# Performance work log

Measured on AMD Instinct MI355X. Metric: run time of the kernel, lower is better.

## Reference

```python
import jax, jax.numpy as jnp
import numpy as np

NUM_HEADS = 12
LN_EPS = 1e-5


def setup_inputs() -> dict:
    key = jax.random.key(0)
    k1, k2, k3 = jax.random.split(key, 3)
    B, S, E = 8, 1024, 768
    x = jax.random.normal(k1, (B, S, E), dtype=jnp.float32)
    # torch nn.Linear(E, 3E): y = x @ W.T + b. We store the transposed weight [E, 3E].
    w_qkv = jax.random.normal(k2, (E, 3 * E), dtype=jnp.float32) * (1.0 / np.sqrt(E))
    b_qkv = jax.random.normal(k3, (3 * E,), dtype=jnp.float32) * 0.02
    ln_gamma = jnp.ones((E,), dtype=jnp.float32)
    ln_beta = jnp.zeros((E,), dtype=jnp.float32)
    return {"x": x, "w_qkv": w_qkv, "b_qkv": b_qkv, "ln_gamma": ln_gamma, "ln_beta": ln_beta}


def reference(x, w_qkv, b_qkv, ln_gamma, ln_beta):
    B, S, E = x.shape
    H = NUM_HEADS
    D = E // H
    qkv = x @ w_qkv + b_qkv                       # [B, S, 3E]
    qkv = qkv.reshape(B, S, 3, H, D)
    q, k, v = qkv[:, :, 0], qkv[:, :, 1], qkv[:, :, 2]   # each [B, S, H, D]
    scores = jnp.einsum("bshd,bthd->bhst", q, k) / jnp.sqrt(jnp.float32(D))
    attn = jax.nn.softmax(scores, axis=-1)        # [B, H, S, S]
    out = jnp.einsum("bhst,bthd->bshd", attn, v)  # [B, S, H, D]
    # per-head concat in head order == reshape to [B, S, E]
    out = out.reshape(B, S, E)
    y = x + out
    mean = jnp.mean(y, axis=-1, keepdims=True)
    var = jnp.var(y, axis=-1, keepdims=True)
    y = (y - mean) * jax.lax.rsqrt(var + LN_EPS)
    return y * ln_gamma + ln_beta
```

## Files before the change

kernel.cpp:

```cpp
#include <hip/hip_runtime.h>

typedef __attribute__((ext_vector_type(8))) short short8;
typedef __attribute__((ext_vector_type(4))) float f32x4;

#define DEVI __device__ __forceinline__

DEVI unsigned fbits(float f) { return __builtin_bit_cast(unsigned, f); }
DEVI unsigned short f2bf(float f) {
    unsigned u = __builtin_bit_cast(unsigned, f);
    u += 0x7fffu + ((u >> 16) & 1u);
    return (unsigned short)(u >> 16);
}
DEVI unsigned pktrunc(float a, float b) {
    return __builtin_amdgcn_perm(fbits(b), fbits(a), 0x07060302u);
}
DEVI void async16(const unsigned short* g, unsigned short* l) {
    __builtin_amdgcn_global_load_lds(
        (const __attribute__((address_space(1))) void*)g,
        (__attribute__((address_space(3))) void*)l,
        16, 0, 0);
}
#define BAR()    asm volatile("s_barrier" ::: "memory")
#define WAITV4() asm volatile("s_waitcnt vmcnt(4)" ::: "memory")
#define WAITV0() asm volatile("s_waitcnt vmcnt(0)" ::: "memory")

__global__ __launch_bounds__(256) void kcvt(const float* __restrict__ x,
                                            unsigned short* __restrict__ xb) {
    const int i = (blockIdx.x * 256 + threadIdx.x) * 4;
    const float4 v = *(const float4*)&x[i];
    uint2 pk;
    pk.x = (unsigned)f2bf(v.x) | ((unsigned)f2bf(v.y) << 16);
    pk.y = (unsigned)f2bf(v.z) | ((unsigned)f2bf(v.w) << 16);
    *(uint2*)&xb[i] = pk;
}

__global__ void ktrans(const float* __restrict__ w,
                       unsigned short* __restrict__ wt) {
    __shared__ float t[32][33];
    const int tx = threadIdx.x, ty = threadIdx.y;
    const int n0 = blockIdx.x * 32, k0 = blockIdx.y * 32;
#pragma unroll
    for (int i = 0; i < 4; i++)
        t[ty + i * 8][tx] = w[(k0 + ty + i * 8) * 2304 + n0 + tx];
    __syncthreads();
#pragma unroll
    for (int i = 0; i < 4; i++)
        wt[(n0 + ty + i * 8) * 768 + k0 + tx] = f2bf(t[tx][ty + i * 8]);
}

__global__ __launch_bounds__(256) void kgemm(
        const unsigned short* __restrict__ xb,
        const unsigned short* __restrict__ wt,
        const float* __restrict__ bias,
        unsigned short* __restrict__ q,
        unsigned short* __restrict__ k_,
        unsigned short* __restrict__ vt) {
    __shared__ __align__(16) unsigned short As[3][8 * 512];
    __shared__ __align__(16) unsigned short Bs[3][8 * 512];
    const int tid = threadIdx.x;
    const int w = tid >> 6, lane = tid & 63;
    const int wm = w >> 1, wn = w & 1;
    const int m0 = blockIdx.y * 128, n0 = blockIdx.x * 128;
    const int gr = lane & 15, gc = (lane >> 4) * 8;

    f32x4 acc[4][4] = {};

    auto issue = [&](int kk, int b) {
#pragma unroll
        for (int j = 0; j < 2; j++) {
            const int t = w + j * 4;
            async16(&xb[(m0 + t * 16 + gr) * 768 + kk + gc], &As[b][t * 512]);
            async16(&wt[(n0 + t * 16 + gr) * 768 + kk + gc], &Bs[b][t * 512]);
        }
    };

    issue(0, 0);
    issue(32, 1);

    for (int it = 0; it < 24; it++) {
        const int cur = it % 3;
        if (it < 23) { WAITV4(); } else { WAITV0(); }
        BAR();
        if (it + 2 < 24) issue((it + 2) * 32, (it + 2) % 3);

        short8 af[4], bf[4];
#pragma unroll
        for (int mi = 0; mi < 4; mi++)
            af[mi] = *(const short8*)&As[cur][(wm * 4 + mi) * 512 + lane * 8];
#pragma unroll
        for (int ni = 0; ni < 4; ni++)
            bf[ni] = *(const short8*)&Bs[cur][(wn * 4 + ni) * 512 + lane * 8];
#pragma unroll
        for (int mi = 0; mi < 4; mi++)
#pragma unroll
            for (int ni = 0; ni < 4; ni++)
                acc[mi][ni] = __builtin_amdgcn_mfma_f32_16x16x32_bf16(
                    af[mi], bf[ni], acc[mi][ni], 0, 0, 0);
    }

    const int col0 = n0 + wn * 64;
    const int row0 = m0 + wm * 64;
#pragma unroll
    for (int mi = 0; mi < 4; mi++) {
#pragma unroll
        for (int ni = 0; ni < 4; ni++) {
            const int n_ = col0 + ni * 16 + (lane & 15);
            const float bv = bias[n_];
            const int which = n_ / 768;
            const int r7 = n_ % 768;
            const int h = r7 >> 6, d = r7 & 63;
#pragma unroll
            for (int r = 0; r < 4; r++) {
                const int m_ = row0 + mi * 16 + (lane >> 4) * 4 + r;
                const int bb = m_ >> 10, s = m_ & 1023;
                const int bh = bb * 12 + h;
                const unsigned short o = f2bf(acc[mi][ni][r] + bv);
                if (which == 0)      q[(bh * 1024 + s) * 64 + d] = o;
                else if (which == 1) k_[(bh * 1024 + s) * 64 + d] = o;
                else                 vt[(bh * 64 + d) * 1024 + s] = o;
            }
        }
    }
}

#define SCL 0.18033688011112042f

__global__ __launch_bounds__(256) void kattn(
        const unsigned short* __restrict__ q,
        const unsigned short* __restrict__ k_,
        const unsigned short* __restrict__ vt,
        float* __restrict__ out) {
    __shared__ __align__(16) unsigned short Ks[2][8 * 512];
    __shared__ __align__(16) unsigned short Vs[2][8 * 512];
    __shared__ __align__(16) unsigned short Ps[4][4 * 512];
    const int tid = threadIdx.x;
    const int w = tid >> 6, lane = tid & 63;
    const int bh = blockIdx.x;
    const int qt = blockIdx.y;
    const int bb = bh / 12, h = bh % 12;
    const unsigned short* qb = q + bh * 1024 * 64;
    const unsigned short* kb = k_ + bh * 1024 * 64;
    const unsigned short* vb = vt + bh * 64 * 1024;

    const int frow = lane & 15;
    const int grp = lane >> 4;
    const int m0 = qt * 128 + w * 32;

    auto issue = [&](int t0, int b) {
#pragma unroll
        for (int j = 0; j < 2; j++) {
            const int t = w * 2 + j, ti = t >> 1, ks = t & 1;
            async16(&kb[(t0 + ti * 16 + frow) * 64 + ks * 32 + grp * 8], &Ks[b][t * 512]);
            async16(&vb[(ti * 16 + frow) * 1024 + t0 + ks * 32 + grp * 8], &Vs[b][t * 512]);
        }
    };

    short8 qf[2][2];
#pragma unroll
    for (int mi = 0; mi < 2; mi++)
#pragma unroll
        for (int ks = 0; ks < 2; ks++)
            qf[mi][ks] = *(const short8*)&qb[(m0 + mi * 16 + frow) * 64 + ks * 32 + grp * 8];

    issue(0, 0);

    f32x4 oacc[2][4] = {};
    float rmax[2] = {-INFINITY, -INFINITY}, rsum[2] = {0.f, 0.f};

    for (int tt = 0; tt < 16; tt++) {
        const int cur = tt & 1;
        WAITV0();
        BAR();
        if (tt + 1 < 16) issue((tt + 1) * 64, cur ^ 1);

        f32x4 sacc[4][2] = {};
#pragma unroll
        for (int ks = 0; ks < 2; ks++) {
            short8 kf[4];
#pragma unroll
            for (int ni = 0; ni < 4; ni++)
                kf[ni] = *(const short8*)&Ks[cur][(ni * 2 + ks) * 512 + lane * 8];
#pragma unroll
            for (int ni = 0; ni < 4; ni++)
#pragma unroll
                for (int mi = 0; mi < 2; mi++)
                    sacc[ni][mi] = __builtin_amdgcn_mfma_f32_16x16x32_bf16(
                        kf[ni], qf[mi][ks], sacc[ni][mi], 0, 0, 0);
        }

#pragma unroll
        for (int mi = 0; mi < 2; mi++) {
            float mt = -INFINITY;
#pragma unroll
            for (int ni = 0; ni < 4; ni++)
#pragma unroll
                for (int r = 0; r < 4; r++) mt = fmaxf(mt, sacc[ni][mi][r]);
            mt = fmaxf(mt, __shfl_xor(mt, 16, 64));
            mt = fmaxf(mt, __shfl_xor(mt, 32, 64));
            const float mnew = fmaxf(rmax[mi], mt);
            const float alpha = exp2f((rmax[mi] - mnew) * SCL);
            rmax[mi] = mnew;
            const float mb = mnew * SCL;
            float ps = 0.f;
#pragma unroll
            for (int ni = 0; ni < 4; ni++)
#pragma unroll
                for (int r = 0; r < 4; r++) {
                    const float p = exp2f(sacc[ni][mi][r] * SCL - mb);
                    sacc[ni][mi][r] = p;
                    ps += p;
                }
            ps += __shfl_xor(ps, 16, 64);
            ps += __shfl_xor(ps, 32, 64);
            rsum[mi] = rsum[mi] * alpha + ps;
#pragma unroll
            for (int di = 0; di < 4; di++) oacc[mi][di] *= alpha;
#pragma unroll
            for (int ni = 0; ni < 4; ni++) {
                uint2 pk;
                pk.x = pktrunc(sacc[ni][mi][0], sacc[ni][mi][1]);
                pk.y = pktrunc(sacc[ni][mi][2], sacc[ni][mi][3]);
                const int dlane = frow + (((ni << 1) + (grp >> 1)) & 3) * 16;
                *(uint2*)&Ps[w][(mi * 2 + (ni >> 1)) * 512 + dlane * 8 + (grp & 1) * 4] = pk;
            }
        }

#pragma unroll
        for (int ks = 0; ks < 2; ks++) {
            short8 vf[4], pf[2];
#pragma unroll
            for (int di = 0; di < 4; di++)
                vf[di] = *(const short8*)&Vs[cur][(di * 2 + ks) * 512 + lane * 8];
#pragma unroll
            for (int mi = 0; mi < 2; mi++)
                pf[mi] = *(const short8*)&Ps[w][(mi * 2 + ks) * 512 + lane * 8];
#pragma unroll
            for (int mi = 0; mi < 2; mi++)
#pragma unroll
                for (int di = 0; di < 4; di++)
                    oacc[mi][di] = __builtin_amdgcn_mfma_f32_16x16x32_bf16(
                        vf[di], pf[mi], oacc[mi][di], 0, 0, 0);
        }
    }

#pragma unroll
    for (int mi = 0; mi < 2; mi++) {
        const float inv = 1.0f / rsum[mi];
        const int s = m0 + mi * 16 + frow;
#pragma unroll
        for (int di = 0; di < 4; di++) {
            f32x4 o = oacc[mi][di] * inv;
            const int d0 = di * 16 + grp * 4;
            *(f32x4*)&out[(bb * 1024 + s) * 768 + h * 64 + d0] = o;
        }
    }
}

__global__ __launch_bounds__(256) void kln(
        const float* __restrict__ x,
        const float* __restrict__ gamma,
        const float* __restrict__ beta,
        float* __restrict__ out) {
    __shared__ float red[8];
    const int row = blockIdx.x;
    const int tid = threadIdx.x;
    const float* xr = x + row * 768;
    float* orow = out + row * 768;
    float y[3], sum = 0.f, sumsq = 0.f;
#pragma unroll
    for (int i = 0; i < 3; i++) {
        const int e = tid + i * 256;
        const float v = xr[e] + orow[e];
        y[i] = v; sum += v; sumsq += v * v;
    }
#pragma unroll
    for (int o = 1; o < 64; o <<= 1) {
        sum += __shfl_xor(sum, o, 64);
        sumsq += __shfl_xor(sumsq, o, 64);
    }
    const int w = tid >> 6, lane = tid & 63;
    if (lane == 0) { red[w] = sum; red[4 + w] = sumsq; }
    __syncthreads();
    sum = red[0] + red[1] + red[2] + red[3];
    sumsq = red[4] + red[5] + red[6] + red[7];
    const float mean = sum * (1.0f / 768.0f);
    const float var = sumsq * (1.0f / 768.0f) - mean * mean;
    const float rs = rsqrtf(var + 1e-5f);
#pragma unroll
    for (int i = 0; i < 3; i++) {
        const int e = tid + i * 256;
        orow[e] = (y[i] - mean) * rs * gamma[e] + beta[e];
    }
}

extern "C" void kernel_launch(void* const* d_in, const int* in_sizes, int n_in,
                              void* d_out, int out_size, void* d_ws, size_t ws_size,
                              hipStream_t stream) {
    (void)in_sizes; (void)n_in; (void)out_size; (void)ws_size;
    const float* x     = (const float*)d_in[0];
    const float* wqkv  = (const float*)d_in[1];
    const float* bqkv  = (const float*)d_in[2];
    const float* gamma = (const float*)d_in[3];
    const float* beta  = (const float*)d_in[4];
    float* out = (float*)d_out;
    unsigned short* ws = (unsigned short*)d_ws;

    unsigned short* wt = ws;
    unsigned short* xb = wt + 2304 * 768;
    unsigned short* q  = xb + 8192 * 768;
    unsigned short* k  = q + 96 * 1024 * 64;
    unsigned short* vt = k + 96 * 1024 * 64;

    kcvt<<<6144, 256, 0, stream>>>(x, xb);
    ktrans<<<dim3(72, 24), dim3(32, 8), 0, stream>>>(wqkv, wt);
    kgemm<<<dim3(18, 64), 256, 0, stream>>>(xb, wt, bqkv, q, k, vt);
    kattn<<<dim3(96, 8), 256, 0, stream>>>(q, k, vt, out);
    kln<<<8192, 256, 0, stream>>>(x, gamma, beta, out);
}
```

Measured before the change: 248.9 us.

## Fuse fp32-to-bf16 conversion of x into GEMM and stage V-transpose through LDS

Removes the separate kcvt kernel. The GEMM now loads fp32 x directly into registers, truncates it to bf16 and writes it into LDS, so the x round trip through a bf16 workspace goes away. The pipeline shrinks from triple-buffered async loads to double buffering with register prefetch of A. The V output tile is transposed through LDS so stores to vt are coalesced 16-byte writes instead of scattered 2-byte stores. Conversion switches from round-to-nearest to truncation, which slightly changes numerics, and the shallower pipeline may expose more memory latency.

Result: no change. 253.5 us (+1.8%).

```diff
diff --git a/kernel.cpp b/kernel.cpp
--- a/kernel.cpp
+++ b/kernel.cpp
@@ -21,18 +21,8 @@
         16, 0, 0);
 }
 #define BAR()    asm volatile("s_barrier" ::: "memory")
-#define WAITV4() asm volatile("s_waitcnt vmcnt(4)" ::: "memory")
+#define BARF()   asm volatile("s_waitcnt lgkmcnt(0)\ns_barrier" ::: "memory")
 #define WAITV0() asm volatile("s_waitcnt vmcnt(0)" ::: "memory")
-
-__global__ __launch_bounds__(256) void kcvt(const float* __restrict__ x,
-                                            unsigned short* __restrict__ xb) {
-    const int i = (blockIdx.x * 256 + threadIdx.x) * 4;
-    const float4 v = *(const float4*)&x[i];
-    uint2 pk;
-    pk.x = (unsigned)f2bf(v.x) | ((unsigned)f2bf(v.y) << 16);
-    pk.y = (unsigned)f2bf(v.z) | ((unsigned)f2bf(v.w) << 16);
-    *(uint2*)&xb[i] = pk;
-}
 
 __global__ void ktrans(const float* __restrict__ w,
                        unsigned short* __restrict__ wt) {
@@ -49,14 +39,13 @@
 }
 
 __global__ __launch_bounds__(256) void kgemm(
-        const unsigned short* __restrict__ xb,
+        const float* __restrict__ A,
         const unsigned short* __restrict__ wt,
         const float* __restrict__ bias,
         unsigned short* __restrict__ q,
         unsigned short* __restrict__ k_,
         unsigned short* __restrict__ vt) {
-    __shared__ __align__(16) unsigned short As[3][8 * 512];
-    __shared__ __align__(16) unsigned short Bs[3][8 * 512];
+    __shared__ __align__(16) unsigned short pool[17408];
     const int tid = threadIdx.x;
     const int w = tid >> 6, lane = tid & 63;
     const int wm = w >> 1, wn = w & 1;
@@ -64,60 +53,109 @@
     const int gr = lane & 15, gc = (lane >> 4) * 8;
 
     f32x4 acc[4][4] = {};
-
-    auto issue = [&](int kk, int b) {
+    float4 a0[2], a1[2];
+
+    auto issueB = [&](int kk, int b) {
 #pragma unroll
         for (int j = 0; j < 2; j++) {
             const int t = w + j * 4;
-            async16(&xb[(m0 + t * 16 + gr) * 768 + kk + gc], &As[b][t * 512]);
-            async16(&wt[(n0 + t * 16 + gr) * 768 + kk + gc], &Bs[b][t * 512]);
+            async16(&wt[(n0 + t * 16 + gr) * 768 + kk + gc],
+                    &pool[8192 + b * 4096 + t * 512 + lane * 8]);
         }
     };
-
-    issue(0, 0);
-    issue(32, 1);
+    auto loadA = [&](int kk) {
+#pragma unroll
+        for (int j = 0; j < 2; j++) {
+            const int t = w + j * 4;
+            const float* p = &A[(m0 + t * 16 + gr) * 768 + kk + gc];
+            a0[j] = *(const float4*)p;
+            a1[j] = *(const float4*)(p + 4);
+        }
+    };
+    auto packA = [&](int b) {
+#pragma unroll
+        for (int j = 0; j < 2; j++) {
+            const int t = w + j * 4;
+            uint4 pk;
+            pk.x = pktrunc(a0[j].x, a0[j].y);
+            pk.y = pktrunc(a0[j].z, a0[j].w);
+            pk.z = pktrunc(a1[j].x, a1[j].y);
+            pk.w = pktrunc(a1[j].z, a1[j].w);
+            *(uint4*)&pool[b * 4096 + t * 512 + lane * 8] = pk;
+        }
+    };
+
+    loadA(0); packA(0); issueB(0, 0);
 
     for (int it = 0; it < 24; it++) {
-        const int cur = it % 3;
-        if (it < 23) { WAITV4(); } else { WAITV0(); }
-        BAR();
-        if (it + 2 < 24) issue((it + 2) * 32, (it + 2) % 3);
+        const int cur = it & 1;
+        WAITV0();
+        BARF();
+        if (it < 23) { issueB((it + 1) * 32, cur ^ 1); loadA((it + 1) * 32); }
 
         short8 af[4], bf[4];
 #pragma unroll
         for (int mi = 0; mi < 4; mi++)
-            af[mi] = *(const short8*)&As[cur][(wm * 4 + mi) * 512 + lane * 8];
+            af[mi] = *(const short8*)&pool[cur * 4096 + (wm * 4 + mi) * 512 + lane * 8];
 #pragma unroll
         for (int ni = 0; ni < 4; ni++)
-            bf[ni] = *(const short8*)&Bs[cur][(wn * 4 + ni) * 512 + lane * 8];
+            bf[ni] = *(const short8*)&pool[8192 + cur * 4096 + (wn * 4 + ni) * 512 + lane * 8];
 #pragma unroll
         for (int mi = 0; mi < 4; mi++)
 #pragma unroll
             for (int ni = 0; ni < 4; ni++)
                 acc[mi][ni] = __builtin_amdgcn_mfma_f32_16x16x32_bf16(
                     af[mi], bf[ni], acc[mi][ni], 0, 0, 0);
-    }
-
-    const int col0 = n0 + wn * 64;
-    const int row0 = m0 + wm * 64;
-#pragma unroll
-    for (int mi = 0; mi < 4; mi++) {
-#pragma unroll
-        for (int ni = 0; ni < 4; ni++) {
-            const int n_ = col0 + ni * 16 + (lane & 15);
-            const float bv = bias[n_];
-            const int which = n_ / 768;
-            const int r7 = n_ % 768;
-            const int h = r7 >> 6, d = r7 & 63;
-#pragma unroll
-            for (int r = 0; r < 4; r++) {
-                const int m_ = row0 + mi * 16 + (lane >> 4) * 4 + r;
-                const int bb = m_ >> 10, s = m_ & 1023;
+
+        if (it < 23) packA(cur ^ 1);
+    }
+
+    const int which = n0 / 768;
+    const int bb = m0 >> 10, sbase = m0 & 1023;
+
+    if (which == 2) {
+        BARF();
+#pragma unroll
+        for (int mi = 0; mi < 4; mi++) {
+            const int mloc = wm * 64 + mi * 16 + (lane >> 4) * 4;
+#pragma unroll
+            for (int ni = 0; ni < 4; ni++) {
+                const int nl = wn * 64 + ni * 16 + gr;
+                const float bv = bias[n0 + nl];
+                uint2 pk;
+                pk.x = pktrunc(acc[mi][ni][0] + bv, acc[mi][ni][1] + bv);
+                pk.y = pktrunc(acc[mi][ni][2] + bv, acc[mi][ni][3] + bv);
+                *(uint2*)&pool[nl * 136 + mloc] = pk;
+            }
+        }
+        BARF();
+        const int h0 = (n0 - 1536) >> 6;
+#pragma unroll
+        for (int cc = 0; cc < 8; cc++) {
+            const int nl = cc * 16 + (tid >> 4);
+            const int mc = (tid & 15) * 8;
+            short8 vv = *(const short8*)&pool[nl * 136 + mc];
+            const int h = h0 + (nl >> 6), d = nl & 63;
+            *(short8*)&vt[((bb * 12 + h) * 64 + d) * 1024 + sbase + mc] = vv;
+        }
+    } else {
+        const int col0 = n0 + wn * 64;
+#pragma unroll
+        for (int mi = 0; mi < 4; mi++) {
+#pragma unroll
+            for (int ni = 0; ni < 4; ni++) {
+                const int n_ = col0 + ni * 16 + gr;
+                const float bv = bias[n_];
+                const int r7 = n_ % 768;
+                const int h = r7 >> 6, d = r7 & 63;
                 const int bh = bb * 12 + h;
-                const unsigned short o = f2bf(acc[mi][ni][r] + bv);
-                if (which == 0)      q[(bh * 1024 + s) * 64 + d] = o;
-                else if (which == 1) k_[(bh * 1024 + s) * 64 + d] = o;
-                else                 vt[(bh * 64 + d) * 1024 + s] = o;
+#pragma unroll
+                for (int r = 0; r < 4; r++) {
+                    const int s = sbase + wm * 64 + mi * 16 + (lane >> 4) * 4 + r;
+                    const unsigned short o = f2bf(acc[mi][ni][r] + bv);
+                    if (which == 0) q[(bh * 1024 + s) * 64 + d] = o;
+                    else            k_[(bh * 1024 + s) * 64 + d] = o;
+                }
             }
         }
     }
@@ -306,14 +344,12 @@
     unsigned short* ws = (unsigned short*)d_ws;
 
     unsigned short* wt = ws;
-    unsigned short* xb = wt + 2304 * 768;
-    unsigned short* q  = xb + 8192 * 768;
+    unsigned short* q  = wt + 2304 * 768;
     unsigned short* k  = q + 96 * 1024 * 64;
     unsigned short* vt = k + 96 * 1024 * 64;
 
-    kcvt<<<6144, 256, 0, stream>>>(x, xb);
     ktrans<<<dim3(72, 24), dim3(32, 8), 0, stream>>>(wqkv, wt);
-    kgemm<<<dim3(18, 64), 256, 0, stream>>>(xb, wt, bqkv, q, k, vt);
+    kgemm<<<dim3(18, 64), 256, 0, stream>>>(x, wt, bqkv, q, k, vt);
     kattn<<<dim3(96, 8), 256, 0, stream>>>(q, k, vt, out);
     kln<<<8192, 256, 0, stream>>>(x, gamma, beta, out);
 }
```
